# Performance work log

Measured on AMD Instinct MI355X. Metric: run time of the kernel, lower is better.

## Reference

```python
import jax, jax.numpy as jnp
import numpy as np

EPS = 1e-16

def setup_inputs() -> dict:
    B, N, M, D = 32, 16384, 128, 1024
    L = 3 * M + 6  # write_lengths sum: k(M), beta(1), g(1), s(3), gamma(1), e(M), a(M)
    ks = jax.random.split(jax.random.key(0), 5)
    embeddings = jax.random.normal(ks[0], (B, D), jnp.float32)
    w_prev = jax.random.uniform(ks[1], (B, N), jnp.float32)
    w_prev = w_prev / jnp.sum(w_prev, axis=1, keepdims=True)  # valid address distribution
    mem = jax.random.normal(ks[2], (B, N, M), jnp.float32) * 0.05
    # Dense params: variance_scaling(1.4, fan_avg, uniform) ~ U(-lim, lim)
    lim = float(np.sqrt(3.0 * 1.4 / ((D + L) / 2.0)))
    W = jax.random.uniform(ks[3], (D, L), jnp.float32, -lim, lim)
    b = jax.random.normal(ks[4], (L,), jnp.float32) * 0.01
    return {"embeddings": embeddings, "w_prev": w_prev, "mem": mem, "W": W, "b": b}

def _forward(embeddings, w_prev, mem, W, b):
    M = mem.shape[-1]
    o = embeddings @ W + b  # [B, 3M+6]
    k = o[:, :M]
    beta = jax.nn.softplus(o[:, M:M + 1])
    g = jax.nn.sigmoid(o[:, M + 1:M + 2])
    s = jax.nn.softmax(o[:, M + 2:M + 5], axis=1)  # 3-tap shift
    gamma = 1.0 + jax.nn.softplus(o[:, M + 5:M + 6])
    e = jax.nn.sigmoid(o[:, M + 6:2 * M + 6])
    a = o[:, 2 * M + 6:]
    # content addressing: cosine similarity -> softmax(beta * sim)
    sim = jnp.einsum('bnm,bm->bn', mem, k) / (
        jnp.linalg.norm(mem, axis=-1) * jnp.linalg.norm(k, axis=-1, keepdims=True) + EPS)
    w_c = jax.nn.softmax(beta * sim, axis=1)
    # interpolation with previous weights
    w_g = g * w_c + (1.0 - g) * w_prev
    # circular convolution with 3-tap shift kernel s = [s(-1), s(0), s(+1)]
    w_t = (s[:, 0:1] * jnp.roll(w_g, 1, axis=1)
           + s[:, 1:2] * w_g
           + s[:, 2:3] * jnp.roll(w_g, -1, axis=1))
    # sharpening
    w_sh = w_t ** gamma
    w = w_sh / (jnp.sum(w_sh, axis=1, keepdims=True) + EPS)
    # erase + add write: mem' = mem * (1 - w e^T) + w a^T
    we = w[:, :, None] * e[:, None, :]  # [B, N, M]
    wa = w[:, :, None] * a[:, None, :]
    new_mem = mem * (1.0 - we) + wa
    return w, new_mem

def reference(embeddings, w_prev, mem, W, b):
    return _forward(embeddings, w_prev, mem, W, b)
```

## Files before the change

kernel.cpp:

```cpp
#include <hip/hip_runtime.h>
#include <math.h>

#define B 32
#define N 16384
#define M 128
#define D 1024
#define L 390
#define EPSF 1e-16f

#define O_OFF  0
#define S1_OFF (B*L)
#define S2_OFF (S1_OFF + B)
#define Z_OFF  (S2_OFF + B)

typedef float fvec4 __attribute__((ext_vector_type(4)));

__device__ __forceinline__ float softplusf(float x) {
    return x > 20.f ? x : log1pf(expf(x));
}
__device__ __forceinline__ float sigmoidf(float x) {
    return 1.f / (1.f + expf(-x));
}

__global__ __launch_bounds__(256) void k1_gemm(const float* __restrict__ emb,
                                               const float* __restrict__ W,
                                               const float* __restrict__ bias,
                                               float* __restrict__ ws) {
    __shared__ float embS[D];
    __shared__ float red[4][64];
    const int l0 = blockIdx.x * 64;
    const int b  = blockIdx.y;
    const int t  = threadIdx.x;
    for (int i = t; i < D; i += 256) embS[i] = emb[b * D + i];
    if (blockIdx.x == 0 && t == 0) {
        ws[S1_OFF + b] = 0.f;
        ws[S2_OFF + b] = 0.f;
    }
    __syncthreads();
    const int li = t & 63;
    const int q  = t >> 6;
    const int l  = l0 + li;
    float partial = 0.f;
    if (l < L) {
        const float* wp = W + (size_t)(q * 256) * L + l;
        #pragma unroll 8
        for (int d = 0; d < 256; ++d) partial += embS[q * 256 + d] * wp[(size_t)d * L];
    }
    red[q][li] = partial;
    __syncthreads();
    if (t < 64 && l0 + t < L) {
        float o = red[0][t] + red[1][t] + red[2][t] + red[3][t] + bias[l0 + t];
        ws[O_OFF + b * L + l0 + t] = o;
    }
}

__global__ __launch_bounds__(256) void k2_sim(const float* __restrict__ mem,
                                              float* __restrict__ ws) {
    const int b = blockIdx.y;
    const int t = threadIdx.x;
    const int n = blockIdx.x * 256 + t;
    const int wave = t >> 6, lane = t & 63;
    __shared__ float kS[M];
    __shared__ float par[2];
    __shared__ float acc[4];
    const float* o = ws + O_OFF + b * L;
    if (t < M) kS[t] = o[t];
    __syncthreads();
    if (t < M) {
        float kv = kS[t];
        float sq = kv * kv;
        #pragma unroll
        for (int off = 32; off >= 1; off >>= 1) sq += __shfl_xor(sq, off, 64);
        if (lane == 0) acc[t >> 6] = sq;
    }
    __syncthreads();
    if (t == 0) {
        par[0] = sqrtf(acc[0] + acc[1]);
        par[1] = softplusf(o[M]);
    }
    __syncthreads();
    const float knorm = par[0], beta = par[1];
    const float* mp = mem + ((size_t)b * N + n) * M;

    float dot = 0.f, sq = 0.f;
    #pragma unroll 16
    for (int j = 0; j < M / 4; ++j) {
        const fvec4 mv = *(const fvec4*)(mp + j * 4);
        const fvec4 kv = *(const fvec4*)&kS[j * 4];
        dot = fmaf(mv.x, kv.x, dot); dot = fmaf(mv.y, kv.y, dot);
        dot = fmaf(mv.z, kv.z, dot); dot = fmaf(mv.w, kv.w, dot);
        sq  = fmaf(mv.x, mv.x, sq);  sq  = fmaf(mv.y, mv.y, sq);
        sq  = fmaf(mv.z, mv.z, sq);  sq  = fmaf(mv.w, mv.w, sq);
    }
    const float sim = dot / (sqrtf(sq) * knorm + EPSF);
    const float uu  = expf(beta * sim);
    ws[Z_OFF + (size_t)b * N + n] = uu;

    float r = uu;
    #pragma unroll
    for (int off = 32; off >= 1; off >>= 1) r += __shfl_xor(r, off, 64);
    if (lane == 0) acc[wave] = r;
    __syncthreads();
    if (t == 0) atomicAdd(ws + S1_OFF + b, acc[0] + acc[1] + acc[2] + acc[3]);
}

__global__ __launch_bounds__(256) void k3_s2(const float* __restrict__ w_prev,
                                             float* __restrict__ ws) {
    const int b = blockIdx.y;
    const int n = blockIdx.x * 256 + threadIdx.x;
    __shared__ float par[6];
    if (threadIdx.x == 0) {
        const float* o = ws + O_OFF + b * L;
        par[0] = sigmoidf(o[M + 1]);
        float x0 = o[M + 2], x1 = o[M + 3], x2 = o[M + 4];
        float mx = fmaxf(x0, fmaxf(x1, x2));
        float e0 = expf(x0 - mx), e1 = expf(x1 - mx), e2 = expf(x2 - mx);
        float inv = 1.f / (e0 + e1 + e2);
        par[1] = e0 * inv; par[2] = e1 * inv; par[3] = e2 * inv;
        par[4] = 1.f + softplusf(o[M + 5]);
        par[5] = 1.f / ws[S1_OFF + b];
    }
    __syncthreads();
    const float g = par[0], s0 = par[1], s1 = par[2], s2 = par[3];
    const float gamma = par[4], invS1 = par[5];
    const float* u  = ws + Z_OFF + (size_t)b * N;
    const float* wp = w_prev + (size_t)b * N;
    const int nm = (n == 0)     ? N - 1 : n - 1;
    const int np = (n == N - 1) ? 0     : n + 1;
    const float gm1 = 1.f - g;
    const float gi  = g * invS1;
    const float wgm = gi * u[nm] + gm1 * wp[nm];
    const float wg0 = gi * u[n ] + gm1 * wp[n ];
    const float wgp = gi * u[np] + gm1 * wp[np];
    const float wt  = s0 * wgm + s1 * wg0 + s2 * wgp;
    const float v = powf(wt, gamma);
    float r = v;
    #pragma unroll
    for (int off = 32; off >= 1; off >>= 1) r += __shfl_xor(r, off, 64);
    __shared__ float acc[4];
    if ((threadIdx.x & 63) == 0) acc[threadIdx.x >> 6] = r;
    __syncthreads();
    if (threadIdx.x == 0) atomicAdd(ws + S2_OFF + b, acc[0] + acc[1] + acc[2] + acc[3]);
}

__global__ __launch_bounds__(256) void k4_write(const float* __restrict__ mem,
                                                const float* __restrict__ w_prev,
                                                const float* __restrict__ ws,
                                                float* __restrict__ out) {
    const int b    = blockIdx.y;
    const int n0   = (gridDim.x - 1 - blockIdx.x) * 64;
    const int t    = threadIdx.x;
    const int wave = t >> 6, lane = t & 63;
    __shared__ float eS[M], aS[M], wS[64];
    __shared__ float par[8];
    const float* o = ws + O_OFF + b * L;
    if (t < M) {
        eS[t] = sigmoidf(o[M + 6 + t]);
        aS[t] = o[2 * M + 6 + t];
    }
    if (t == 0) {
        par[0] = sigmoidf(o[M + 1]);
        float x0 = o[M + 2], x1 = o[M + 3], x2 = o[M + 4];
        float mx = fmaxf(x0, fmaxf(x1, x2));
        float e0 = expf(x0 - mx), e1 = expf(x1 - mx), e2 = expf(x2 - mx);
        float inv = 1.f / (e0 + e1 + e2);
        par[1] = e0 * inv; par[2] = e1 * inv; par[3] = e2 * inv;
        par[4] = 1.f + softplusf(o[M + 5]);
        par[5] = 1.f / ws[S1_OFF + b];
        par[6] = 1.f / (ws[S2_OFF + b] + EPSF);
    }
    __syncthreads();
    if (t < 64) {
        const int n  = n0 + t;
        const float g = par[0], s0 = par[1], s1v = par[2], s2v = par[3];
        const float gamma = par[4], invS1 = par[5], invS2 = par[6];
        const float gi = g * invS1, gm1 = 1.f - g;
        const float* u  = ws + Z_OFF + (size_t)b * N;
        const float* wp = w_prev + (size_t)b * N;
        const int nm = (n == 0)     ? N - 1 : n - 1;
        const int np = (n == N - 1) ? 0     : n + 1;
        const float wgm = gi * u[nm] + gm1 * wp[nm];
        const float wg0 = gi * u[n ] + gm1 * wp[n ];
        const float wgp = gi * u[np] + gm1 * wp[np];
        const float wt  = s0 * wgm + s1v * wg0 + s2v * wgp;
        const float wv  = powf(wt, gamma) * invS2;
        wS[t] = wv;
        out[(size_t)b * N + n] = wv;
    }
    __syncthreads();
    float* m_out = out + (size_t)B * N;
    const int col  = (lane & 31) * 4;
    const int half = lane >> 5;
    const fvec4 ev = *(const fvec4*)&eS[col];
    const fvec4 av = *(const fvec4*)&aS[col];
    #pragma unroll
    for (int it = 0; it < 8; ++it) {
        const int loc = wave * 16 + it * 2 + half;
        const int n   = n0 + loc;
        const float w = wS[loc];
        const size_t idx = ((size_t)b * N + n) * M + col;
        const fvec4 mv = *(const fvec4*)(mem + idx);
        fvec4 r;
        r.x = fmaf(mv.x, fmaf(-w, ev.x, 1.f), w * av.x);
        r.y = fmaf(mv.y, fmaf(-w, ev.y, 1.f), w * av.y);
        r.z = fmaf(mv.z, fmaf(-w, ev.z, 1.f), w * av.z);
        r.w = fmaf(mv.w, fmaf(-w, ev.w, 1.f), w * av.w);
        *(fvec4*)(m_out + idx) = r;
    }
}

extern "C" void kernel_launch(void* const* d_in, const int* in_sizes, int n_in,
                              void* d_out, int out_size, void* d_ws, size_t ws_size,
                              hipStream_t stream) {
    const float* emb    = (const float*)d_in[0];
    const float* w_prev = (const float*)d_in[1];
    const float* mem    = (const float*)d_in[2];
    const float* W      = (const float*)d_in[3];
    const float* bias   = (const float*)d_in[4];
    float* ws  = (float*)d_ws;
    float* out = (float*)d_out;

    k1_gemm <<<dim3(7, B),       256, 0, stream>>>(emb, W, bias, ws);
    k2_sim  <<<dim3(N / 256, B), 256, 0, stream>>>(mem, ws);
    k3_s2   <<<dim3(N / 256, B), 256, 0, stream>>>(w_prev, ws);
    k4_write<<<dim3(N / 64, B),  256, 0, stream>>>(mem, w_prev, ws, out);
}
```

Measured before the change: 546.6 us.

## Assign one memory row per thread in write kernel with nontemporal stores

Restructures the erase/add write kernel so each thread computes its own address weight and then streams its entire 128-float memory row, removing the shared-memory weight staging and second barrier. Grid is reduced to 256 rows per block, and output stores use nontemporal hints to avoid cache pollution. The per-thread row layout makes each wave's vector loads stride across 64 separate rows, which risks poor coalescing.

```diff
diff --git a/kernel.cpp b/kernel.cpp
--- a/kernel.cpp
+++ b/kernel.cpp
@@ -147,11 +147,10 @@
                                                 const float* __restrict__ w_prev,
                                                 const float* __restrict__ ws,
                                                 float* __restrict__ out) {
-    const int b    = blockIdx.y;
-    const int n0   = (gridDim.x - 1 - blockIdx.x) * 64;
-    const int t    = threadIdx.x;
-    const int wave = t >> 6, lane = t & 63;
-    __shared__ float eS[M], aS[M], wS[64];
+    const int b  = blockIdx.y;
+    const int n0 = (gridDim.x - 1 - blockIdx.x) * 256;
+    const int t  = threadIdx.x;
+    __shared__ float eS[M], aS[M];
     __shared__ float par[8];
     const float* o = ws + O_OFF + b * L;
     if (t < M) {
@@ -170,8 +169,9 @@
         par[6] = 1.f / (ws[S2_OFF + b] + EPSF);
     }
     __syncthreads();
-    if (t < 64) {
-        const int n  = n0 + t;
+
+    const int n = n0 + t;
+    {
         const float g = par[0], s0 = par[1], s1v = par[2], s2v = par[3];
         const float gamma = par[4], invS1 = par[5], invS2 = par[6];
         const float gi = g * invS1, gm1 = 1.f - g;
@@ -183,29 +183,48 @@
         const float wg0 = gi * u[n ] + gm1 * wp[n ];
         const float wgp = gi * u[np] + gm1 * wp[np];
         const float wt  = s0 * wgm + s1v * wg0 + s2v * wgp;
-        const float wv  = powf(wt, gamma) * invS2;
-        wS[t] = wv;
-        out[(size_t)b * N + n] = wv;
-    }
-    __syncthreads();
-    float* m_out = out + (size_t)B * N;
-    const int col  = (lane & 31) * 4;
-    const int half = lane >> 5;
-    const fvec4 ev = *(const fvec4*)&eS[col];
-    const fvec4 av = *(const fvec4*)&aS[col];
-    #pragma unroll
-    for (int it = 0; it < 8; ++it) {
-        const int loc = wave * 16 + it * 2 + half;
-        const int n   = n0 + loc;
-        const float w = wS[loc];
-        const size_t idx = ((size_t)b * N + n) * M + col;
-        const fvec4 mv = *(const fvec4*)(mem + idx);
-        fvec4 r;
-        r.x = fmaf(mv.x, fmaf(-w, ev.x, 1.f), w * av.x);
-        r.y = fmaf(mv.y, fmaf(-w, ev.y, 1.f), w * av.y);
-        r.z = fmaf(mv.z, fmaf(-w, ev.z, 1.f), w * av.z);
-        r.w = fmaf(mv.w, fmaf(-w, ev.w, 1.f), w * av.w);
-        *(fvec4*)(m_out + idx) = r;
+        const float w   = powf(wt, gamma) * invS2;
+        out[(size_t)b * N + n] = w;
+
+        const size_t ro = ((size_t)b * N + n) * M;
+        const float* src = mem + ro;
+        float*       dst = out + (size_t)B * N + ro;
+        #pragma unroll
+        for (int j0 = 0; j0 < M / 4; j0 += 4) {
+            const fvec4 v0 = *(const fvec4*)(src + (j0 + 0) * 4);
+            const fvec4 v1 = *(const fvec4*)(src + (j0 + 1) * 4);
+            const fvec4 v2 = *(const fvec4*)(src + (j0 + 2) * 4);
+            const fvec4 v3 = *(const fvec4*)(src + (j0 + 3) * 4);
+            const fvec4 e0 = *(const fvec4*)&eS[(j0 + 0) * 4];
+            const fvec4 e1 = *(const fvec4*)&eS[(j0 + 1) * 4];
+            const fvec4 e2 = *(const fvec4*)&eS[(j0 + 2) * 4];
+            const fvec4 e3 = *(const fvec4*)&eS[(j0 + 3) * 4];
+            const fvec4 a0 = *(const fvec4*)&aS[(j0 + 0) * 4];
+            const fvec4 a1 = *(const fvec4*)&aS[(j0 + 1) * 4];
+            const fvec4 a2 = *(const fvec4*)&aS[(j0 + 2) * 4];
+            const fvec4 a3 = *(const fvec4*)&aS[(j0 + 3) * 4];
+            fvec4 r0, r1, r2, r3;
+            r0.x = fmaf(v0.x, fmaf(-w, e0.x, 1.f), w * a0.x);
+            r0.y = fmaf(v0.y, fmaf(-w, e0.y, 1.f), w * a0.y);
+            r0.z = fmaf(v0.z, fmaf(-w, e0.z, 1.f), w * a0.z);
+            r0.w = fmaf(v0.w, fmaf(-w, e0.w, 1.f), w * a0.w);
+            r1.x = fmaf(v1.x, fmaf(-w, e1.x, 1.f), w * a1.x);
+            r1.y = fmaf(v1.y, fmaf(-w, e1.y, 1.f), w * a1.y);
+            r1.z = fmaf(v1.z, fmaf(-w, e1.z, 1.f), w * a1.z);
+            r1.w = fmaf(v1.w, fmaf(-w, e1.w, 1.f), w * a1.w);
+            r2.x = fmaf(v2.x, fmaf(-w, e2.x, 1.f), w * a2.x);
+            r2.y = fmaf(v2.y, fmaf(-w, e2.y, 1.f), w * a2.y);
+            r2.z = fmaf(v2.z, fmaf(-w, e2.z, 1.f), w * a2.z);
+            r2.w = fmaf(v2.w, fmaf(-w, e2.w, 1.f), w * a2.w);
+            r3.x = fmaf(v3.x, fmaf(-w, e3.x, 1.f), w * a3.x);
+            r3.y = fmaf(v3.y, fmaf(-w, e3.y, 1.f), w * a3.y);
+            r3.z = fmaf(v3.z, fmaf(-w, e3.z, 1.f), w * a3.z);
+            r3.w = fmaf(v3.w, fmaf(-w, e3.w, 1.f), w * a3.w);
+            __builtin_nontemporal_store(r0, (fvec4*)(dst + (j0 + 0) * 4));
+            __builtin_nontemporal_store(r1, (fvec4*)(dst + (j0 + 1) * 4));
+            __builtin_nontemporal_store(r2, (fvec4*)(dst + (j0 + 2) * 4));
+            __builtin_nontemporal_store(r3, (fvec4*)(dst + (j0 + 3) * 4));
+        }
     }
 }
 
@@ -223,5 +242,5 @@
     k1_gemm <<<dim3(7, B),       256, 0, stream>>>(emb, W, bias, ws);
     k2_sim  <<<dim3(N / 256, B), 256, 0, stream>>>(mem, ws);
     k3_s2   <<<dim3(N / 256, B), 256, 0, stream>>>(w_prev, ws);
-    k4_write<<<dim3(N / 64, B),  256, 0, stream>>>(mem, w_prev, ws, out);
-}
+    k4_write<<<dim3(N / 256, B), 256, 0, stream>>>(mem, w_prev, ws, out);
+}
```

New measurement: 1.018 ms. 1.86x slower.
